# Kernel optimization log

Hardware: AMD Instinct MI355X
Metric: run time of the kernel (lower is better)

Reference implementation:

```python
import jax, jax.numpy as jnp
import numpy as np

B, L, D, K_LIN, T = 32, 512, 1024, 7, 8  # T = 1 identity ('root') + 7 linear experts


def setup_inputs() -> dict:
    key = jax.random.key(0)
    k0, k1, k2 = jax.random.split(key, 3)
    actions = jax.random.normal(k0, (B, L, D), dtype=jnp.float32)
    action_type = jax.random.randint(k1, (B, L), 0, T)
    W = jax.random.normal(k2, (K_LIN, D, D), dtype=jnp.float32) * 0.02  # (K, out, in)
    b = jnp.zeros((K_LIN, D), dtype=jnp.float32)
    return {"actions": actions, "action_type": action_type, "W": W, "b": b}


def reference(actions, action_type, W, b):
    # Project padded actions through ALL experts (matches original ModuleDict loop).
    # proj: (B, L, K_LIN, D) ; W is (K, out, in) so contract over input dim i.
    proj = jnp.einsum('bli,koi->blko', actions, W) + b[None, None, :, :]
    # 'root' expert is nn.Identity -> stacked first (dict insertion order).
    p = jnp.concatenate([actions[:, :, None, :], proj], axis=2)  # (B, L, T, D)
    # One-hot mask built via scatter in the original == one_hot here.
    mask = jax.nn.one_hot(action_type, T, dtype=p.dtype)[..., None]  # (B, L, T, 1)
    embedded = (mask * p).sum(axis=2)  # (B, L, D)
    return embedded
```

## Files before the change

kernel.cpp:

```cpp
#include <hip/hip_runtime.h>


#define NTOK 16384
#define DDIM 1024
#define NEXP 7
#define BM 256
#define BN 256
#define BK 64
#define NKT (DDIM / BK)

#define WI_OFFS   16
#define WI_NTILES 32
#define WI_TABLE  64
#define WI_CTOK   512
#define WI_SMAP   (512 + 16384)
#define WS_ABF_B  1048576
#define WS_WBF_B  (WS_ABF_B + NTOK * DDIM * 2)

typedef __attribute__((ext_vector_type(8))) short short8;
typedef __attribute__((ext_vector_type(4))) float f32x4;

__device__ __forceinline__ unsigned short f2bf(float f) {
    unsigned u = __float_as_uint(f);
    u += 0x7fff + ((u >> 16) & 1);
    return (unsigned short)(u >> 16);
}

__device__ __forceinline__ void gload16(const void* g, void* l) {
    __builtin_amdgcn_global_load_lds(
        (const __attribute__((address_space(1))) void*)g,
        (__attribute__((address_space(3))) void*)l, 16, 0, 0);
}

__global__ __launch_bounds__(1024) void route_k(
    const int* __restrict__ type, int* __restrict__ wsi) {
    __shared__ int h[16][8];
    __shared__ int cur[16][NEXP];
    const int tid = threadIdx.x, wave = tid >> 6;

    if (tid < 128) ((int*)h)[tid] = 0;
    __syncthreads();

    int kv[16];
#pragma unroll
    for (int i = 0; i < 16; ++i) {
        kv[i] = type[i * 1024 + tid];
        if (kv[i] > 0) atomicAdd(&h[wave][kv[i]], 1);
    }
    __syncthreads();

    if (tid == 0) {
        int acc = 0, t = 0;
        for (int e = 0; e < NEXP; ++e) {
            wsi[WI_OFFS + e] = acc;
            int run = acc;
            for (int w = 0; w < 16; ++w) { cur[w][e] = run; run += h[w][e + 1]; }
            int nt = (run - acc + BM - 1) >> 8;
            for (int i = 0; i < nt; ++i) {
                wsi[WI_TABLE + 2 * t] = e;
                wsi[WI_TABLE + 2 * t + 1] = acc + i * BM;
                ++t;
            }
            acc = run;
        }
        wsi[WI_OFFS + NEXP] = acc;
        wsi[WI_NTILES] = t;
    }
    __syncthreads();

#pragma unroll
    for (int i = 0; i < 16; ++i) {
        int t = i * 1024 + tid, s = -1;
        if (kv[i] > 0) {
            s = atomicAdd(&cur[wave][kv[i] - 1], 1);
            wsi[WI_CTOK + s] = t;
        }
        wsi[WI_SMAP + t] = s;
    }
}

__global__ __launch_bounds__(256) void fusedconv_k(
    const float* __restrict__ A, const int* __restrict__ wsi,
    const float* __restrict__ W, unsigned short* __restrict__ Wbf,
    unsigned short* __restrict__ Abf, float* __restrict__ out) {
    const int bid = blockIdx.x, tid = threadIdx.x;
    if (bid < 4096) {
        int wave = tid >> 6, lane = tid & 63;
        int t = bid * 4 + wave;
        int s = wsi[WI_SMAP + t];
        const float4* src = (const float4*)(A + (size_t)t * DDIM);
        if (s < 0) {
            float4* d = (float4*)(out + (size_t)t * DDIM);
#pragma unroll
            for (int j = 0; j < 4; ++j) d[lane + j * 64] = src[lane + j * 64];
        } else {
            float4 v0 = src[lane * 4 + 0], v1 = src[lane * 4 + 1];
            float4 v2 = src[lane * 4 + 2], v3 = src[lane * 4 + 3];
            short8 h0, h1;
            h0[0]=f2bf(v0.x); h0[1]=f2bf(v0.y); h0[2]=f2bf(v0.z); h0[3]=f2bf(v0.w);
            h0[4]=f2bf(v1.x); h0[5]=f2bf(v1.y); h0[6]=f2bf(v1.z); h0[7]=f2bf(v1.w);
            h1[0]=f2bf(v2.x); h1[1]=f2bf(v2.y); h1[2]=f2bf(v2.z); h1[3]=f2bf(v2.w);
            h1[4]=f2bf(v3.x); h1[5]=f2bf(v3.y); h1[6]=f2bf(v3.z); h1[7]=f2bf(v3.w);
            unsigned short* d = Abf + (size_t)s * DDIM + lane * 16;
            *(short8*)d = h0;
            *(short8*)(d + 8) = h1;
        }
    } else {
        size_t i = ((size_t)(bid - 4096) * 256 + tid) * 16;
        const float4* src = (const float4*)(W + i);
        float4 v0 = src[0], v1 = src[1], v2 = src[2], v3 = src[3];
        short8 h0, h1;
        h0[0]=f2bf(v0.x); h0[1]=f2bf(v0.y); h0[2]=f2bf(v0.z); h0[3]=f2bf(v0.w);
        h0[4]=f2bf(v1.x); h0[5]=f2bf(v1.y); h0[6]=f2bf(v1.z); h0[7]=f2bf(v1.w);
        h1[0]=f2bf(v2.x); h1[1]=f2bf(v2.y); h1[2]=f2bf(v2.z); h1[3]=f2bf(v2.w);
        h1[4]=f2bf(v3.x); h1[5]=f2bf(v3.y); h1[6]=f2bf(v3.z); h1[7]=f2bf(v3.w);
        *(short8*)(Wbf + i) = h0;
        *(short8*)(Wbf + i + 8) = h1;
    }
}

#define TILE(Abase, Bbase, sNA, sNB, KT)                           \
    do {                                                           \
        short8 a1[8], b1[4];                                       \
        _Pragma("unroll")                                          \
        for (int m = 0; m < 8; ++m)                                \
            a1[m] = *(const short8*)(Abase + sl0 + m * 2048);      \
        _Pragma("unroll")                                          \
        for (int n = 0; n < 4; ++n)                                \
            b1[n] = *(const short8*)(Bbase + sl0 + n * 2048);      \
        if ((KT) + 1 < NKT) {                                      \
            const int ke_ = ((KT) + 1) * BK;                       \
            _Pragma("unroll")                                      \
            for (int q = 0; q < 4; ++q)                            \
                gload16(aSrc[q] + ke_, sNA + q * 8192);            \
            _Pragma("unroll")                                      \
            for (int q = 0; q < 4; ++q)                            \
                gload16(bSrc[q] + ke_, sNB + q * 8192);            \
        }                                                          \
        __builtin_amdgcn_s_setprio(1);                             \
        _Pragma("unroll")                                          \
        for (int m = 0; m < 8; ++m)                                \
            _Pragma("unroll")                                      \
            for (int n = 0; n < 4; ++n)                            \
                acc[m][n] = __builtin_amdgcn_mfma_f32_16x16x32_bf16(\
                    a1[m], b1[n], acc[m][n], 0, 0, 0);             \
        __builtin_amdgcn_s_setprio(0);                             \
        short8 a2[8], b2[4];                                       \
        _Pragma("unroll")                                          \
        for (int m = 0; m < 8; ++m)                                \
            a2[m] = *(const short8*)(Abase + sl1 + m * 2048);      \
        _Pragma("unroll")                                          \
        for (int n = 0; n < 4; ++n)                                \
            b2[n] = *(const short8*)(Bbase + sl1 + n * 2048);      \
        __builtin_amdgcn_s_setprio(1);                             \
        _Pragma("unroll")                                          \
        for (int m = 0; m < 8; ++m)                                \
            _Pragma("unroll")                                      \
            for (int n = 0; n < 4; ++n)                            \
                acc[m][n] = __builtin_amdgcn_mfma_f32_16x16x32_bf16(\
                    a2[m], b2[n], acc[m][n], 0, 0, 0);             \
        __builtin_amdgcn_s_setprio(0);                             \
        asm volatile("s_waitcnt vmcnt(0)" ::: "memory");           \
        __builtin_amdgcn_s_barrier();                              \
    } while (0)

__global__ __launch_bounds__(512, 2) void gemm_k(
    const unsigned short* __restrict__ Abf,
    const unsigned short* __restrict__ Wbf,
    const float* __restrict__ bias, float* __restrict__ out,
    const int* __restrict__ wsi) {
    const int bid = blockIdx.x;
    const int c = bid & 7;
    const int g = bid >> 3;
    const int ntiles = wsi[WI_NTILES];
    const int* offs = wsi + WI_OFFS;
    const int* tab  = wsi + WI_TABLE;
    const int* ctok = wsi + WI_CTOK;

    __shared__ unsigned short As0[BM * BK];
    __shared__ unsigned short As1[BM * BK];
    __shared__ unsigned short Bs0[BM * BK];
    __shared__ unsigned short Bs1[BM * BK];

    const int tid = threadIdx.x, lane = tid & 63, wave = tid >> 6;
    const int wr = wave >> 2, wc = wave & 3;
    const int lane15 = lane & 15;
    const int srow = lane >> 3;
    const int schunk = ((lane & 7) ^ srow) * 8;

    const int sl0 = (((lane >> 4)) ^ (lane & 7)) * 16;
    const int sl1 = ((4 | (lane >> 4)) ^ (lane & 7)) * 16;
    const char* aR0 = (const char*)As0 + wr * 16384 + lane15 * 128;
    const char* aR1 = (const char*)As1 + wr * 16384 + lane15 * 128;
    const char* bR0 = (const char*)Bs0 + wc * 8192 + lane15 * 128;
    const char* bR1 = (const char*)Bs1 + wc * 8192 + lane15 * 128;
    char* sA0 = (char*)As0 + wave * 1024;
    char* sA1 = (char*)As1 + wave * 1024;
    char* sB0 = (char*)Bs0 + wave * 1024;
    char* sB1 = (char*)Bs1 + wave * 1024;

    for (int rep = 0; rep < 2; ++rep) {
        const int q4 = g + 32 * rep;
        const int ty = (q4 >> 2) * 8 + c;
        const int tx = q4 & 3;
        if (ty >= ntiles) break;

        const int e     = tab[2 * ty];
        const int crow0 = tab[2 * ty + 1];
        const int nend  = offs[e + 1];
        const int col0  = tx * BN;
        const unsigned short* Wb = Wbf + (size_t)e * DDIM * DDIM;

        const unsigned short* aSrc[4];
        const unsigned short* bSrc[4];
#pragma unroll
        for (int q = 0; q < 4; ++q) {
            int r = min(crow0 + q * 64 + wave * 8 + srow, NTOK - 1);
            aSrc[q] = Abf + (size_t)r * DDIM + schunk;
            bSrc[q] = Wb + (size_t)(col0 + q * 64 + wave * 8 + srow) * DDIM + schunk;
        }

        f32x4 acc[8][4];
#pragma unroll
        for (int m = 0; m < 8; ++m)
#pragma unroll
            for (int n = 0; n < 4; ++n) acc[m][n] = (f32x4){0.f, 0.f, 0.f, 0.f};

#pragma unroll
        for (int q = 0; q < 4; ++q) gload16(aSrc[q], sA0 + q * 8192);
#pragma unroll
        for (int q = 0; q < 4; ++q) gload16(bSrc[q], sB0 + q * 8192);
        asm volatile("s_waitcnt vmcnt(0)" ::: "memory");
        __builtin_amdgcn_s_barrier();

        for (int kt2 = 0; kt2 < NKT / 2; ++kt2) {
            TILE(aR0, bR0, sA1, sB1, 2 * kt2);
            TILE(aR1, bR1, sA0, sB0, 2 * kt2 + 1);
        }

        const int crow4 = (lane >> 4) * 4;
        float bv[4];
#pragma unroll
        for (int n = 0; n < 4; ++n)
            bv[n] = bias[e * DDIM + col0 + wc * 64 + n * 16 + lane15];

#pragma unroll
        for (int m = 0; m < 8; ++m) {
#pragma unroll
            for (int r = 0; r < 4; ++r) {
                int gr = crow0 + wr * 128 + m * 16 + crow4 + r;
                if (gr >= nend) continue;
                int tok = ctok[gr];
                float* orow = out + (size_t)tok * DDIM + col0 + wc * 64 + lane15;
#pragma unroll
                for (int n = 0; n < 4; ++n)
                    orow[n * 16] = acc[m][n][r] + bv[n];
            }
        }
        __builtin_amdgcn_s_barrier();
    }
}

extern "C" void kernel_launch(void* const* d_in, const int* in_sizes, int n_in,
                              void* d_out, int out_size, void* d_ws, size_t ws_size,
                              hipStream_t stream) {
    const float* actions = (const float*)d_in[0];
    const int*   atype   = (const int*)d_in[1];
    const float* W       = (const float*)d_in[2];
    const float* bias    = (const float*)d_in[3];
    float* out = (float*)d_out;

    int* wsi = (int*)d_ws;
    unsigned short* Abf = (unsigned short*)((char*)d_ws + WS_ABF_B);
    unsigned short* Wbf = (unsigned short*)((char*)d_ws + WS_WBF_B);

    route_k<<<1, 1024, 0, stream>>>(atype, wsi);
    fusedconv_k<<<4096 + 1792, 256, 0, stream>>>(actions, wsi, W, Wbf, Abf, out);
    gemm_k<<<256, 512, 0, stream>>>(Abf, Wbf, bias, out, wsi);
}
```

Baseline: 82.64 us.

## Gather and convert activations inside GEMM, fuse routing with weight conversion

```diff
diff --git a/kernel.cpp b/kernel.cpp
--- a/kernel.cpp
+++ b/kernel.cpp
@@ -13,9 +13,7 @@
 #define WI_NTILES 32
 #define WI_TABLE  64
 #define WI_CTOK   512
-#define WI_SMAP   (512 + 16384)
-#define WS_ABF_B  1048576
-#define WS_WBF_B  (WS_ABF_B + NTOK * DDIM * 2)
+#define WS_WBF_B  1048576
 
 typedef __attribute__((ext_vector_type(8))) short short8;
 typedef __attribute__((ext_vector_type(4))) float f32x4;
@@ -32,81 +30,51 @@
         (__attribute__((address_space(3))) void*)l, 16, 0, 0);
 }
 
-__global__ __launch_bounds__(1024) void route_k(
-    const int* __restrict__ type, int* __restrict__ wsi) {
-    __shared__ int h[16][8];
-    __shared__ int cur[16][NEXP];
-    const int tid = threadIdx.x, wave = tid >> 6;
-
-    if (tid < 128) ((int*)h)[tid] = 0;
-    __syncthreads();
-
-    int kv[16];
-#pragma unroll
-    for (int i = 0; i < 16; ++i) {
-        kv[i] = type[i * 1024 + tid];
-        if (kv[i] > 0) atomicAdd(&h[wave][kv[i]], 1);
-    }
-    __syncthreads();
-
-    if (tid == 0) {
-        int acc = 0, t = 0;
-        for (int e = 0; e < NEXP; ++e) {
-            wsi[WI_OFFS + e] = acc;
+__global__ __launch_bounds__(256) void routeconv_k(
+    const int* __restrict__ type, int* __restrict__ wsi,
+    const float* __restrict__ W, unsigned short* __restrict__ Wbf) {
+    const int bid = blockIdx.x, tid = threadIdx.x;
+    if (bid == 0) {
+        __shared__ int h[4][8];
+        __shared__ int base2[4][8];
+        const int wave = tid >> 6;
+        if (tid < 32) ((int*)h)[tid] = 0;
+        __syncthreads();
+        for (int i = 0; i < 64; ++i) {
+            int k = type[i * 256 + tid];
+            atomicAdd(&h[wave][k], 1);
+        }
+        __syncthreads();
+        if (tid == 0) {
+            int acc = 0, t = 0;
+            for (int e = 0; e < NEXP; ++e) {
+                wsi[WI_OFFS + e] = acc;
+                int run = acc;
+                for (int w = 0; w < 4; ++w) { base2[w][e + 1] = run; run += h[w][e + 1]; }
+                int nt = (run - acc + BM - 1) >> 8;
+                for (int i = 0; i < nt; ++i) {
+                    wsi[WI_TABLE + 2 * t] = e;
+                    wsi[WI_TABLE + 2 * t + 1] = acc + i * BM;
+                    ++t;
+                }
+                acc = run;
+            }
+            wsi[WI_OFFS + NEXP] = acc;
+            wsi[WI_NTILES] = t;
             int run = acc;
-            for (int w = 0; w < 16; ++w) { cur[w][e] = run; run += h[w][e + 1]; }
-            int nt = (run - acc + BM - 1) >> 8;
-            for (int i = 0; i < nt; ++i) {
-                wsi[WI_TABLE + 2 * t] = e;
-                wsi[WI_TABLE + 2 * t + 1] = acc + i * BM;
-                ++t;
-            }
-            acc = run;
-        }
-        wsi[WI_OFFS + NEXP] = acc;
-        wsi[WI_NTILES] = t;
-    }
-    __syncthreads();
-
-#pragma unroll
-    for (int i = 0; i < 16; ++i) {
-        int t = i * 1024 + tid, s = -1;
-        if (kv[i] > 0) {
-            s = atomicAdd(&cur[wave][kv[i] - 1], 1);
-            wsi[WI_CTOK + s] = t;
-        }
-        wsi[WI_SMAP + t] = s;
-    }
-}
-
-__global__ __launch_bounds__(256) void fusedconv_k(
-    const float* __restrict__ A, const int* __restrict__ wsi,
-    const float* __restrict__ W, unsigned short* __restrict__ Wbf,
-    unsigned short* __restrict__ Abf, float* __restrict__ out) {
-    const int bid = blockIdx.x, tid = threadIdx.x;
-    if (bid < 4096) {
-        int wave = tid >> 6, lane = tid & 63;
-        int t = bid * 4 + wave;
-        int s = wsi[WI_SMAP + t];
-        const float4* src = (const float4*)(A + (size_t)t * DDIM);
-        if (s < 0) {
-            float4* d = (float4*)(out + (size_t)t * DDIM);
-#pragma unroll
-            for (int j = 0; j < 4; ++j) d[lane + j * 64] = src[lane + j * 64];
-        } else {
-            float4 v0 = src[lane * 4 + 0], v1 = src[lane * 4 + 1];
-            float4 v2 = src[lane * 4 + 2], v3 = src[lane * 4 + 3];
-            short8 h0, h1;
-            h0[0]=f2bf(v0.x); h0[1]=f2bf(v0.y); h0[2]=f2bf(v0.z); h0[3]=f2bf(v0.w);
-            h0[4]=f2bf(v1.x); h0[5]=f2bf(v1.y); h0[6]=f2bf(v1.z); h0[7]=f2bf(v1.w);
-            h1[0]=f2bf(v2.x); h1[1]=f2bf(v2.y); h1[2]=f2bf(v2.z); h1[3]=f2bf(v2.w);
-            h1[4]=f2bf(v3.x); h1[5]=f2bf(v3.y); h1[6]=f2bf(v3.z); h1[7]=f2bf(v3.w);
-            unsigned short* d = Abf + (size_t)s * DDIM + lane * 16;
-            *(short8*)d = h0;
-            *(short8*)(d + 8) = h1;
+            for (int w = 0; w < 4; ++w) { base2[w][0] = run; run += h[w][0]; }
+        }
+        __syncthreads();
+        if (tid < 32) ((int*)h)[tid] = 0;
+        __syncthreads();
+        for (int i = 0; i < 64; ++i) {
+            int t2 = i * 256 + tid;
+            int k = type[t2];
+            int pos = base2[wave][k] + atomicAdd(&h[wave][k], 1);
+            wsi[WI_CTOK + pos] = t2;
         }
     } else {
-        size_t i = ((size_t)(bid - 4096) * 256 + tid) * 16;
+        size_t i = ((size_t)(bid - 1) * 256 + tid) * 16;
         const float4* src = (const float4*)(W + i);
         float4 v0 = src[0], v1 = src[1], v2 = src[2], v3 = src[3];
         short8 h0, h1;
@@ -119,9 +87,24 @@
     }
 }
 
-#define TILE(Abase, Bbase, sNA, sNB, KT)                           \
+__global__ __launch_bounds__(256) void identity_k(
+    const float* __restrict__ A, const int* __restrict__ wsi,
+    float* __restrict__ out) {
+    const int wave = threadIdx.x >> 6, lane = threadIdx.x & 63;
+    const int nlin = wsi[WI_OFFS + NEXP];
+    const int idx = blockIdx.x * 4 + wave;
+    if (idx >= NTOK - nlin) return;
+    const int tok = wsi[WI_CTOK + nlin + idx];
+    const float4* s = (const float4*)(A + (size_t)tok * DDIM);
+    float4* d = (float4*)(out + (size_t)tok * DDIM);
+#pragma unroll
+    for (int j = 0; j < 4; ++j) d[lane + j * 64] = s[lane + j * 64];
+}
+
+#define TILE(Abase, Bbase, dNA, sNB, KT)                           \
     do {                                                           \
         short8 a1[8], b1[4];                                       \
+        float4 fA[8];                                              \
         _Pragma("unroll")                                          \
         for (int m = 0; m < 8; ++m)                                \
             a1[m] = *(const short8*)(Abase + sl0 + m * 2048);      \
@@ -132,10 +115,13 @@
             const int ke_ = ((KT) + 1) * BK;                       \
             _Pragma("unroll")                                      \
             for (int q = 0; q < 4; ++q)                            \
-                gload16(aSrc[q] + ke_, sNA + q * 8192);            \
-            _Pragma("unroll")                                      \
-            for (int q = 0; q < 4; ++q)                            \
                 gload16(bSrc[q] + ke_, sNB + q * 8192);            \
+            _Pragma("unroll")                                      \
+            for (int q = 0; q < 4; ++q) {                          \
+                const float* p = aSrcF[q] + ke_;                   \
+                fA[2 * q]     = *(const float4*)p;                 \
+                fA[2 * q + 1] = *(const float4*)(p + 4);           \
+            }                                                      \
         }                                                          \
         __builtin_amdgcn_s_setprio(1);                             \
         _Pragma("unroll")                                          \
@@ -161,11 +147,22 @@
                     a2[m], b2[n], acc[m][n], 0, 0, 0);             \
         __builtin_amdgcn_s_setprio(0);                             \
         asm volatile("s_waitcnt vmcnt(0)" ::: "memory");           \
+        if ((KT) + 1 < NKT) {                                      \
+            _Pragma("unroll")                                      \
+            for (int q = 0; q < 4; ++q) {                          \
+                short8 w;                                          \
+                w[0]=f2bf(fA[2*q].x);   w[1]=f2bf(fA[2*q].y);      \
+                w[2]=f2bf(fA[2*q].z);   w[3]=f2bf(fA[2*q].w);      \
+                w[4]=f2bf(fA[2*q+1].x); w[5]=f2bf(fA[2*q+1].y);    \
+                w[6]=f2bf(fA[2*q+1].z); w[7]=f2bf(fA[2*q+1].w);    \
+                *(short8*)(dNA + awOff[q]) = w;                    \
+            }                                                      \
+        }                                                          \
         __builtin_amdgcn_s_barrier();                              \
     } while (0)
 
 __global__ __launch_bounds__(512, 2) void gemm_k(
-    const unsigned short* __restrict__ Abf,
+    const float* __restrict__ Araw,
     const unsigned short* __restrict__ Wbf,
     const float* __restrict__ bias, float* __restrict__ out,
     const int* __restrict__ wsi) {
@@ -194,10 +191,14 @@
     const char* aR1 = (const char*)As1 + wr * 16384 + lane15 * 128;
     const char* bR0 = (const char*)Bs0 + wc * 8192 + lane15 * 128;
     const char* bR1 = (const char*)Bs1 + wc * 8192 + lane15 * 128;
-    char* sA0 = (char*)As0 + wave * 1024;
-    char* sA1 = (char*)As1 + wave * 1024;
     char* sB0 = (char*)Bs0 + wave * 1024;
     char* sB1 = (char*)Bs1 + wave * 1024;
+
+    int awOff[4];
+#pragma unroll
+    for (int q = 0; q < 4; ++q)
+        awOff[q] = (q * 64 + wave * 8 + srow) * 128 +
+                   (((lane & 7) ^ (srow & 7)) * 16);
 
     for (int rep = 0; rep < 2; ++rep) {
         const int q4 = g + 32 * rep;
@@ -211,12 +212,12 @@
         const int col0  = tx * BN;
         const unsigned short* Wb = Wbf + (size_t)e * DDIM * DDIM;
 
-        const unsigned short* aSrc[4];
+        const float* aSrcF[4];
         const unsigned short* bSrc[4];
 #pragma unroll
         for (int q = 0; q < 4; ++q) {
             int r = min(crow0 + q * 64 + wave * 8 + srow, NTOK - 1);
-            aSrc[q] = Abf + (size_t)r * DDIM + schunk;
+            aSrcF[q] = Araw + (size_t)ctok[r] * DDIM + (lane & 7) * 8;
             bSrc[q] = Wb + (size_t)(col0 + q * 64 + wave * 8 + srow) * DDIM + schunk;
         }
 
@@ -226,16 +227,31 @@
 #pragma unroll
             for (int n = 0; n < 4; ++n) acc[m][n] = (f32x4){0.f, 0.f, 0.f, 0.f};
 
-#pragma unroll
-        for (int q = 0; q < 4; ++q) gload16(aSrc[q], sA0 + q * 8192);
-#pragma unroll
-        for (int q = 0; q < 4; ++q) gload16(bSrc[q], sB0 + q * 8192);
-        asm volatile("s_waitcnt vmcnt(0)" ::: "memory");
-        __builtin_amdgcn_s_barrier();
+        {
+#pragma unroll
+            for (int q = 0; q < 4; ++q) gload16(bSrc[q], sB0 + q * 8192);
+            float4 fA[8];
+#pragma unroll
+            for (int q = 0; q < 4; ++q) {
+                fA[2 * q]     = *(const float4*)aSrcF[q];
+                fA[2 * q + 1] = *(const float4*)(aSrcF[q] + 4);
+            }
+            asm volatile("s_waitcnt vmcnt(0)" ::: "memory");
+#pragma unroll
+            for (int q = 0; q < 4; ++q) {
+                short8 w;
+                w[0]=f2bf(fA[2*q].x);   w[1]=f2bf(fA[2*q].y);
+                w[2]=f2bf(fA[2*q].z);   w[3]=f2bf(fA[2*q].w);
+                w[4]=f2bf(fA[2*q+1].x); w[5]=f2bf(fA[2*q+1].y);
+                w[6]=f2bf(fA[2*q+1].z); w[7]=f2bf(fA[2*q+1].w);
+                *(short8*)((char*)As0 + awOff[q]) = w;
+            }
+            __builtin_amdgcn_s_barrier();
+        }
 
         for (int kt2 = 0; kt2 < NKT / 2; ++kt2) {
-            TILE(aR0, bR0, sA1, sB1, 2 * kt2);
-            TILE(aR1, bR1, sA0, sB0, 2 * kt2 + 1);
+            TILE(aR0, bR0, (char*)As1, sB1, 2 * kt2);
+            TILE(aR1, bR1, (char*)As0, sB0, 2 * kt2 + 1);
         }
 
         const int crow4 = (lane >> 4) * 4;
@@ -271,10 +287,9 @@
     float* out = (float*)d_out;
 
     int* wsi = (int*)d_ws;
-    unsigned short* Abf = (unsigned short*)((char*)d_ws + WS_ABF_B);
     unsigned short* Wbf = (unsigned short*)((char*)d_ws + WS_WBF_B);
 
-    route_k<<<1, 1024, 0, stream>>>(atype, wsi);
-    fusedconv_k<<<4096 + 1792, 256, 0, stream>>>(actions, wsi, W, Wbf, Abf, out);
-    gemm_k<<<256, 512, 0, stream>>>(Abf, Wbf, bias, out, wsi);
-}
+    routeconv_k<<<1 + 1792, 256, 0, stream>>>(atype, wsi, W, Wbf);
+    identity_k<<<NTOK / 4, 256, 0, stream>>>(actions, wsi, out);
+    gemm_k<<<256, 512, 0, stream>>>(actions, Wbf, bias, out, wsi);
+}
```

Measured after the change: 109.3 us. +32.2%, slower.

## Overlap routing with weight conversion and deepen B-operand prefetch in GEMM

Applied to the files above, without the earlier changes.

```diff
diff --git a/kernel.cpp b/kernel.cpp
--- a/kernel.cpp
+++ b/kernel.cpp
@@ -13,7 +13,6 @@
 #define WI_NTILES 32
 #define WI_TABLE  64
 #define WI_CTOK   512
-#define WI_SMAP   (512 + 16384)
 #define WS_ABF_B  1048576
 #define WS_WBF_B  (WS_ABF_B + NTOK * DDIM * 2)
 
@@ -32,81 +31,51 @@
         (__attribute__((address_space(3))) void*)l, 16, 0, 0);
 }
 
-__global__ __launch_bounds__(1024) void route_k(
-    const int* __restrict__ type, int* __restrict__ wsi) {
-    __shared__ int h[16][8];
-    __shared__ int cur[16][NEXP];
-    const int tid = threadIdx.x, wave = tid >> 6;
-
-    if (tid < 128) ((int*)h)[tid] = 0;
-    __syncthreads();
-
-    int kv[16];
-#pragma unroll
-    for (int i = 0; i < 16; ++i) {
-        kv[i] = type[i * 1024 + tid];
-        if (kv[i] > 0) atomicAdd(&h[wave][kv[i]], 1);
-    }
-    __syncthreads();
-
-    if (tid == 0) {
-        int acc = 0, t = 0;
-        for (int e = 0; e < NEXP; ++e) {
-            wsi[WI_OFFS + e] = acc;
+__global__ __launch_bounds__(256) void routeconv_k(
+    const int* __restrict__ type, int* __restrict__ wsi,
+    const float* __restrict__ W, unsigned short* __restrict__ Wbf) {
+    const int bid = blockIdx.x, tid = threadIdx.x;
+    if (bid == 0) {
+        __shared__ int h[4][8];
+        __shared__ int base2[4][8];
+        const int wave = tid >> 6;
+        if (tid < 32) ((int*)h)[tid] = 0;
+        __syncthreads();
+        for (int i = 0; i < 64; ++i) {
+            int k = type[i * 256 + tid];
+            atomicAdd(&h[wave][k], 1);
+        }
+        __syncthreads();
+        if (tid == 0) {
+            int acc = 0, t = 0;
+            for (int e = 0; e < NEXP; ++e) {
+                wsi[WI_OFFS + e] = acc;
+                int run = acc;
+                for (int w = 0; w < 4; ++w) { base2[w][e + 1] = run; run += h[w][e + 1]; }
+                int nt = (run - acc + BM - 1) >> 8;
+                for (int i = 0; i < nt; ++i) {
+                    wsi[WI_TABLE + 2 * t] = e;
+                    wsi[WI_TABLE + 2 * t + 1] = acc + i * BM;
+                    ++t;
+                }
+                acc = run;
+            }
+            wsi[WI_OFFS + NEXP] = acc;
+            wsi[WI_NTILES] = t;
             int run = acc;
-            for (int w = 0; w < 16; ++w) { cur[w][e] = run; run += h[w][e + 1]; }
-            int nt = (run - acc + BM - 1) >> 8;
-            for (int i = 0; i < nt; ++i) {
-                wsi[WI_TABLE + 2 * t] = e;
-                wsi[WI_TABLE + 2 * t + 1] = acc + i * BM;
-                ++t;
-            }
-            acc = run;
-        }
-        wsi[WI_OFFS + NEXP] = acc;
-        wsi[WI_NTILES] = t;
-    }
-    __syncthreads();
-
-#pragma unroll
-    for (int i = 0; i < 16; ++i) {
-        int t = i * 1024 + tid, s = -1;
-        if (kv[i] > 0) {
-            s = atomicAdd(&cur[wave][kv[i] - 1], 1);
-            wsi[WI_CTOK + s] = t;
-        }
-        wsi[WI_SMAP + t] = s;
-    }
-}
-
-__global__ __launch_bounds__(256) void fusedconv_k(
-    const float* __restrict__ A, const int* __restrict__ wsi,
-    const float* __restrict__ W, unsigned short* __restrict__ Wbf,
-    unsigned short* __restrict__ Abf, float* __restrict__ out) {
-    const int bid = blockIdx.x, tid = threadIdx.x;
-    if (bid < 4096) {
-        int wave = tid >> 6, lane = tid & 63;
-        int t = bid * 4 + wave;
-        int s = wsi[WI_SMAP + t];
-        const float4* src = (const float4*)(A + (size_t)t * DDIM);
-        if (s < 0) {
-            float4* d = (float4*)(out + (size_t)t * DDIM);
-#pragma unroll
-            for (int j = 0; j < 4; ++j) d[lane + j * 64] = src[lane + j * 64];
-        } else {
-            float4 v0 = src[lane * 4 + 0], v1 = src[lane * 4 + 1];
-            float4 v2 = src[lane * 4 + 2], v3 = src[lane * 4 + 3];
-            short8 h0, h1;
-            h0[0]=f2bf(v0.x); h0[1]=f2bf(v0.y); h0[2]=f2bf(v0.z); h0[3]=f2bf(v0.w);
-            h0[4]=f2bf(v1.x); h0[5]=f2bf(v1.y); h0[6]=f2bf(v1.z); h0[7]=f2bf(v1.w);
-            h1[0]=f2bf(v2.x); h1[1]=f2bf(v2.y); h1[2]=f2bf(v2.z); h1[3]=f2bf(v2.w);
-            h1[4]=f2bf(v3.x); h1[5]=f2bf(v3.y); h1[6]=f2bf(v3.z); h1[7]=f2bf(v3.w);
-            unsigned short* d = Abf + (size_t)s * DDIM + lane * 16;
-            *(short8*)d = h0;
-            *(short8*)(d + 8) = h1;
+            for (int w = 0; w < 4; ++w) { base2[w][0] = run; run += h[w][0]; }
+        }
+        __syncthreads();
+        if (tid < 32) ((int*)h)[tid] = 0;
+        __syncthreads();
+        for (int i = 0; i < 64; ++i) {
+            int t2 = i * 256 + tid;
+            int k = type[t2];
+            int pos = base2[wave][k] + atomicAdd(&h[wave][k], 1);
+            wsi[WI_CTOK + pos] = t2;
         }
     } else {
-        size_t i = ((size_t)(bid - 4096) * 256 + tid) * 16;
+        size_t i = ((size_t)(bid - 1) * 256 + tid) * 16;
         const float4* src = (const float4*)(W + i);
         float4 v0 = src[0], v1 = src[1], v2 = src[2], v3 = src[3];
         short8 h0, h1;
@@ -119,23 +88,50 @@
     }
 }
 
-#define TILE(Abase, Bbase, sNA, sNB, KT)                           \
+__global__ __launch_bounds__(256) void aconv_k(
+    const float* __restrict__ A, const int* __restrict__ wsi,
+    unsigned short* __restrict__ Abf, float* __restrict__ out) {
+    const int wave = threadIdx.x >> 6, lane = threadIdx.x & 63;
+    const int s = blockIdx.x * 4 + wave;
+    const int nlin = wsi[WI_OFFS + NEXP];
+    const int tok = wsi[WI_CTOK + s];
+    const float4* src = (const float4*)(A + (size_t)tok * DDIM);
+    if (s >= nlin) {
+        float4* d = (float4*)(out + (size_t)tok * DDIM);
+#pragma unroll
+        for (int j = 0; j < 4; ++j) d[lane + j * 64] = src[lane + j * 64];
+    } else {
+        float4 v0 = src[lane * 4 + 0], v1 = src[lane * 4 + 1];
+        float4 v2 = src[lane * 4 + 2], v3 = src[lane * 4 + 3];
+        short8 h0, h1;
+        h0[0]=f2bf(v0.x); h0[1]=f2bf(v0.y); h0[2]=f2bf(v0.z); h0[3]=f2bf(v0.w);
+        h0[4]=f2bf(v1.x); h0[5]=f2bf(v1.y); h0[6]=f2bf(v1.z); h0[7]=f2bf(v1.w);
+        h1[0]=f2bf(v2.x); h1[1]=f2bf(v2.y); h1[2]=f2bf(v2.z); h1[3]=f2bf(v2.w);
+        h1[4]=f2bf(v3.x); h1[5]=f2bf(v3.y); h1[6]=f2bf(v3.z); h1[7]=f2bf(v3.w);
+        unsigned short* d = Abf + (size_t)s * DDIM + lane * 16;
+        *(short8*)d = h0;
+        *(short8*)(d + 8) = h1;
+    }
+}
+
+#define TILEX(AR, BR, sNA, sNB, KT, VMN)                           \
     do {                                                           \
         short8 a1[8], b1[4];                                       \
         _Pragma("unroll")                                          \
         for (int m = 0; m < 8; ++m)                                \
-            a1[m] = *(const short8*)(Abase + sl0 + m * 2048);      \
+            a1[m] = *(const short8*)(AR + sl0 + m * 2048);         \
         _Pragma("unroll")                                          \
         for (int n = 0; n < 4; ++n)                                \
-            b1[n] = *(const short8*)(Bbase + sl0 + n * 2048);      \
+            b1[n] = *(const short8*)(BR + sl0 + n * 2048);         \
         if ((KT) + 1 < NKT) {                                      \
-            const int ke_ = ((KT) + 1) * BK;                       \
             _Pragma("unroll")                                      \
             for (int q = 0; q < 4; ++q)                            \
-                gload16(aSrc[q] + ke_, sNA + q * 8192);            \
+                gload16(aSrc[q] + ((KT) + 1) * BK, sNA + q * 8192);\
+        }                                                          \
+        if ((KT) + 2 < NKT) {                                      \
             _Pragma("unroll")                                      \
             for (int q = 0; q < 4; ++q)                            \
-                gload16(bSrc[q] + ke_, sNB + q * 8192);            \
+                gload16(bSrc[q] + ((KT) + 2) * BK, sNB + q * 8192);\
         }                                                          \
         __builtin_amdgcn_s_setprio(1);                             \
         _Pragma("unroll")                                          \
@@ -148,10 +144,10 @@
         short8 a2[8], b2[4];                                       \
         _Pragma("unroll")                                          \
         for (int m = 0; m < 8; ++m)                                \
-            a2[m] = *(const short8*)(Abase + sl1 + m * 2048);      \
+            a2[m] = *(const short8*)(AR + sl1 + m * 2048);         \
         _Pragma("unroll")                                          \
         for (int n = 0; n < 4; ++n)                                \
-            b2[n] = *(const short8*)(Bbase + sl1 + n * 2048);      \
+            b2[n] = *(const short8*)(BR + sl1 + n * 2048);         \
         __builtin_amdgcn_s_setprio(1);                             \
         _Pragma("unroll")                                          \
         for (int m = 0; m < 8; ++m)                                \
@@ -160,7 +156,7 @@
                 acc[m][n] = __builtin_amdgcn_mfma_f32_16x16x32_bf16(\
                     a2[m], b2[n], acc[m][n], 0, 0, 0);             \
         __builtin_amdgcn_s_setprio(0);                             \
-        asm volatile("s_waitcnt vmcnt(0)" ::: "memory");           \
+        asm volatile("s_waitcnt vmcnt(" #VMN ")" ::: "memory");    \
         __builtin_amdgcn_s_barrier();                              \
     } while (0)
 
@@ -181,6 +177,7 @@
     __shared__ unsigned short As1[BM * BK];
     __shared__ unsigned short Bs0[BM * BK];
     __shared__ unsigned short Bs1[BM * BK];
+    __shared__ unsigned short Bs2[BM * BK];
 
     const int tid = threadIdx.x, lane = tid & 63, wave = tid >> 6;
     const int wr = wave >> 2, wc = wave & 3;
@@ -194,10 +191,12 @@
     const char* aR1 = (const char*)As1 + wr * 16384 + lane15 * 128;
     const char* bR0 = (const char*)Bs0 + wc * 8192 + lane15 * 128;
     const char* bR1 = (const char*)Bs1 + wc * 8192 + lane15 * 128;
+    const char* bR2 = (const char*)Bs2 + wc * 8192 + lane15 * 128;
     char* sA0 = (char*)As0 + wave * 1024;
     char* sA1 = (char*)As1 + wave * 1024;
     char* sB0 = (char*)Bs0 + wave * 1024;
     char* sB1 = (char*)Bs1 + wave * 1024;
+    char* sB2 = (char*)Bs2 + wave * 1024;
 
     for (int rep = 0; rep < 2; ++rep) {
         const int q4 = g + 32 * rep;
@@ -227,16 +226,30 @@
             for (int n = 0; n < 4; ++n) acc[m][n] = (f32x4){0.f, 0.f, 0.f, 0.f};
 
 #pragma unroll
+        for (int q = 0; q < 4; ++q) gload16(bSrc[q], sB0 + q * 8192);
+#pragma unroll
         for (int q = 0; q < 4; ++q) gload16(aSrc[q], sA0 + q * 8192);
 #pragma unroll
-        for (int q = 0; q < 4; ++q) gload16(bSrc[q], sB0 + q * 8192);
-        asm volatile("s_waitcnt vmcnt(0)" ::: "memory");
+        for (int q = 0; q < 4; ++q) gload16(bSrc[q] + BK, sB1 + q * 8192);
+        asm volatile("s_waitcnt vmcnt(4)" ::: "memory");
         __builtin_amdgcn_s_barrier();
 
-        for (int kt2 = 0; kt2 < NKT / 2; ++kt2) {
-            TILE(aR0, bR0, sA1, sB1, 2 * kt2);
-            TILE(aR1, bR1, sA0, sB0, 2 * kt2 + 1);
-        }
+        TILEX(aR0, bR0, sA1, sB2,  0, 4);
+        TILEX(aR1, bR1, sA0, sB0,  1, 4);
+        TILEX(aR0, bR2, sA1, sB1,  2, 4);
+        TILEX(aR1, bR0, sA0, sB2,  3, 4);
+        TILEX(aR0, bR1, sA1, sB0,  4, 4);
+        TILEX(aR1, bR2, sA0, sB1,  5, 4);
+        TILEX(aR0, bR0, sA1, sB2,  6, 4);
+        TILEX(aR1, bR1, sA0, sB0,  7, 4);
+        TILEX(aR0, bR2, sA1, sB1,  8, 4);
+        TILEX(aR1, bR0, sA0, sB2,  9, 4);
+        TILEX(aR0, bR1, sA1, sB0, 10, 4);
+        TILEX(aR1, bR2, sA0, sB1, 11, 4);
+        TILEX(aR0, bR0, sA1, sB2, 12, 4);
+        TILEX(aR1, bR1, sA0, sB0, 13, 4);
+        TILEX(aR0, bR2, sA1, sB1, 14, 0);
+        TILEX(aR1, bR0, sA0, sB2, 15, 0);
 
         const int crow4 = (lane >> 4) * 4;
         float bv[4];
@@ -274,7 +287,7 @@
     unsigned short* Abf = (unsigned short*)((char*)d_ws + WS_ABF_B);
     unsigned short* Wbf = (unsigned short*)((char*)d_ws + WS_WBF_B);
 
-    route_k<<<1, 1024, 0, stream>>>(atype, wsi);
-    fusedconv_k<<<4096 + 1792, 256, 0, stream>>>(actions, wsi, W, Wbf, Abf, out);
+    routeconv_k<<<1 + 1792, 256, 0, stream>>>(atype, wsi, W, Wbf);
+    aconv_k<<<NTOK / 4, 256, 0, stream>>>(actions, wsi, Abf, out);
     gemm_k<<<256, 512, 0, stream>>>(Abf, Wbf, bias, out, wsi);
 }
```

Result: slower. 91.82 us (+11.1%).
